# Kernel optimization log

Hardware: AMD Instinct MI355X
Metric: run time of the kernel (lower is better)

The kernel has to match this reference:

```python
import jax, jax.numpy as jnp
import numpy as np

IN_FEATURES = 8192
OUT_FEATURES = 8192
PACKED_ROWS = IN_FEATURES // 1024 * 96  # 3 uint32 words per 32 int3 values


def unpack_int3(qweight):
    """Unpack GPTQ int3 layout: each group of 3 uint32 words along the row axis
    encodes 32 int3 values for 32 consecutive in-features (per output column).
    Matches Quant3Linear.pack():
      word0: v0..v9 at bits 0,3,...,27; low 2 bits of v10 at bits 30-31
      word1: bit0 = high bit of v10; v11..v20 at bits 1,4,...,28; bit31 = low bit of v21
      word2: bits 0-1 = high 2 bits of v21; v22..v31 at bits 2,5,...,29
    Returns float32 array of shape (in_features, out_features).
    """
    out_f = qweight.shape[-1]
    q = qweight.astype(jnp.uint32).reshape(-1, 3, out_f)  # (groups, 3, out)
    w0, w1, w2 = q[:, 0], q[:, 1], q[:, 2]
    seven = jnp.uint32(7)
    vals = []
    for j in range(10):
        vals.append((w0 >> (3 * j)) & seven)
    vals.append(((w0 >> 30) & jnp.uint32(3)) | ((w1 & jnp.uint32(1)) << 2))  # v10
    for j in range(10):
        vals.append((w1 >> (3 * j + 1)) & seven)
    vals.append(((w1 >> 31) & jnp.uint32(1)) | ((w2 & jnp.uint32(3)) << 1))  # v21
    for j in range(10):
        vals.append((w2 >> (3 * j + 2)) & seven)
    w = jnp.stack(vals, axis=1)  # (groups, 32, out)
    return w.reshape(-1, out_f).astype(jnp.float32)  # (in, out)


def setup_inputs() -> dict:
    key = jax.random.key(0)
    k_x, k_q, k_s, k_z, k_b = jax.random.split(key, 5)
    x = jax.random.normal(k_x, (1, IN_FEATURES), dtype=jnp.float32)
    # random packed bits (full 32-bit entropy), stored as int32 like the torch buffer
    qweight = jax.random.bits(k_q, (PACKED_ROWS, OUT_FEATURES), dtype=jnp.uint32).astype(jnp.int32)
    scales = jax.random.uniform(k_s, (OUT_FEATURES, 1), dtype=jnp.float32, minval=0.01, maxval=0.05)
    # buffer stores zeros*scales (already pre-multiplied in pack())
    zeros = jax.random.uniform(k_z, (OUT_FEATURES, 1), dtype=jnp.float32, minval=0.0, maxval=0.2)
    bias = jax.random.normal(k_b, (OUT_FEATURES,), dtype=jnp.float32)
    return {"x": x, "qweight": qweight, "scales": scales, "zeros": zeros, "bias": bias}


def reference(x, qweight, scales, zeros, bias):
    # y[o] = bias[o] + sum_i x[i] * (scales[o] * q[i,o] - zeros[o])
    dtype = x.dtype
    q = unpack_int3(qweight)                      # (in, out) float32
    W = q * scales.T - zeros.T                    # dequantized weight (in, out)
    y = x.astype(jnp.float32) @ W + bias          # (1, out)
    return y.astype(dtype)
```

## Files before the change

### kernel.cpp

```cpp
#include <hip/hip_runtime.h>
#include <cstdint>

#define IN_F 8192
#define OUT_F 8192
#define KCHUNKS 32
#define ROWS_PER_CHUNK 24
#define KB_PER_CHUNK 8
#define COLS_PER_BLOCK 256

__global__ __launch_bounds__(256) void q3gemv(
    const float* __restrict__ x, const uint32_t* __restrict__ qw,
    const float* __restrict__ scales, const float* __restrict__ zeros,
    const float* __restrict__ bias, float* __restrict__ out)
{
    __shared__ float red[4];

    const int tid = threadIdx.x;
    const int col = blockIdx.x * COLS_PER_BLOCK + tid;
    const int kc  = blockIdx.y;

    float xv = x[kc * 256 + tid];
    float s = xv;
    #pragma unroll
    for (int off = 32; off > 0; off >>= 1)
        s += __shfl_down(s, off, 64);
    const int wid  = tid >> 6;
    const int lane = tid & 63;
    if (lane == 0) red[wid] = s;
    __syncthreads();
    const float sx_slice = red[0] + red[1] + red[2] + red[3];

    const uint32_t* qp = qw + (size_t)(kc * ROWS_PER_CHUNK) * OUT_F + col;
    const float* xb = x + kc * 256;
    float a0 = 0.f, a1 = 0.f, a2 = 0.f, a3 = 0.f;

    #pragma unroll
    for (int kb = 0; kb < KB_PER_CHUNK; ++kb) {
        const uint32_t w0 = qp[0];
        const uint32_t w1 = qp[OUT_F];
        const uint32_t w2 = qp[2 * OUT_F];
        qp += 3 * OUT_F;
        const float* xs = xb + kb * 32;

        a0 += xs[0]  * (float)( w0         & 7u);
        a1 += xs[1]  * (float)((w0 >> 3)   & 7u);
        a2 += xs[2]  * (float)((w0 >> 6)   & 7u);
        a3 += xs[3]  * (float)((w0 >> 9)   & 7u);
        a0 += xs[4]  * (float)((w0 >> 12)  & 7u);
        a1 += xs[5]  * (float)((w0 >> 15)  & 7u);
        a2 += xs[6]  * (float)((w0 >> 18)  & 7u);
        a3 += xs[7]  * (float)((w0 >> 21)  & 7u);
        a0 += xs[8]  * (float)((w0 >> 24)  & 7u);
        a1 += xs[9]  * (float)((w0 >> 27)  & 7u);
        a2 += xs[10] * (float)(((w0 >> 30) & 3u) | ((w1 & 1u) << 2));
        a3 += xs[11] * (float)((w1 >> 1)   & 7u);
        a0 += xs[12] * (float)((w1 >> 4)   & 7u);
        a1 += xs[13] * (float)((w1 >> 7)   & 7u);
        a2 += xs[14] * (float)((w1 >> 10)  & 7u);
        a3 += xs[15] * (float)((w1 >> 13)  & 7u);
        a0 += xs[16] * (float)((w1 >> 16)  & 7u);
        a1 += xs[17] * (float)((w1 >> 19)  & 7u);
        a2 += xs[18] * (float)((w1 >> 22)  & 7u);
        a3 += xs[19] * (float)((w1 >> 25)  & 7u);
        a0 += xs[20] * (float)((w1 >> 28)  & 7u);
        a1 += xs[21] * (float)(((w1 >> 31) & 1u) | ((w2 & 3u) << 1));
        a2 += xs[22] * (float)((w2 >> 2)   & 7u);
        a3 += xs[23] * (float)((w2 >> 5)   & 7u);
        a0 += xs[24] * (float)((w2 >> 8)   & 7u);
        a1 += xs[25] * (float)((w2 >> 11)  & 7u);
        a2 += xs[26] * (float)((w2 >> 14)  & 7u);
        a3 += xs[27] * (float)((w2 >> 17)  & 7u);
        a0 += xs[28] * (float)((w2 >> 20)  & 7u);
        a1 += xs[29] * (float)((w2 >> 23)  & 7u);
        a2 += xs[30] * (float)((w2 >> 26)  & 7u);
        a3 += xs[31] * (float)((w2 >> 29)  & 7u);
    }

    const float dot = (a0 + a1) + (a2 + a3);
    float v = scales[col] * dot - zeros[col] * sx_slice;
    if (kc == 0) v += bias[col];
    atomicAdd(&out[col], v);
}

extern "C" void kernel_launch(void* const* d_in, const int* in_sizes, int n_in,
                              void* d_out, int out_size, void* d_ws, size_t ws_size,
                              hipStream_t stream) {
    const float*    x      = (const float*)d_in[0];
    const uint32_t* qw     = (const uint32_t*)d_in[1];
    const float*    scales = (const float*)d_in[2];
    const float*    zeros  = (const float*)d_in[3];
    const float*    bias   = (const float*)d_in[4];
    float* out = (float*)d_out;

    hipMemsetAsync(out, 0, OUT_F * sizeof(float), stream);

    dim3 grid(OUT_F / COLS_PER_BLOCK, KCHUNKS);
    q3gemv<<<grid, 256, 0, stream>>>(x, qw, scales, zeros, bias, out);
}
```

Measured before the change: 79.69 us.

## Vectorize weight loads to four columns per thread and split K into more chunks

Each thread now handles four adjacent output columns and loads packed weights as uint4 (128-bit) loads. The K dimension is split into 64 chunks of 128 inputs instead of 32 chunks of 256, which keeps the block count the same. The per-chunk sum of x is computed with a single-wavefront xor shuffle, with no shared memory or barrier. The aim is wider memory transactions and more x reuse per thread. The costs are a single accumulator chain per column, twice as many atomics per output, and more registers per thread.

```diff
diff --git a/kernel.cpp b/kernel.cpp
--- a/kernel.cpp
+++ b/kernel.cpp
@@ -3,83 +3,97 @@
 
 #define IN_F 8192
 #define OUT_F 8192
-#define KCHUNKS 32
-#define ROWS_PER_CHUNK 24
-#define KB_PER_CHUNK 8
-#define COLS_PER_BLOCK 256
+#define KCHUNKS 64
+#define ROWS_PER_CHUNK 12
+#define KB_PER_CHUNK 4
+#define THREADS 256
+#define COLS_PER_THREAD 4
+#define COLS_PER_BLOCK (THREADS * COLS_PER_THREAD)
 
-__global__ __launch_bounds__(256) void q3gemv(
+__device__ __forceinline__ void unpack_fma(uint32_t w0, uint32_t w1, uint32_t w2,
+                                           const float* __restrict__ xs, float& a)
+{
+    a += xs[0]  * (float)( w0         & 7u);
+    a += xs[1]  * (float)((w0 >> 3)   & 7u);
+    a += xs[2]  * (float)((w0 >> 6)   & 7u);
+    a += xs[3]  * (float)((w0 >> 9)   & 7u);
+    a += xs[4]  * (float)((w0 >> 12)  & 7u);
+    a += xs[5]  * (float)((w0 >> 15)  & 7u);
+    a += xs[6]  * (float)((w0 >> 18)  & 7u);
+    a += xs[7]  * (float)((w0 >> 21)  & 7u);
+    a += xs[8]  * (float)((w0 >> 24)  & 7u);
+    a += xs[9]  * (float)((w0 >> 27)  & 7u);
+    a += xs[10] * (float)(((w0 >> 30) & 3u) | ((w1 & 1u) << 2));
+    a += xs[11] * (float)((w1 >> 1)   & 7u);
+    a += xs[12] * (float)((w1 >> 4)   & 7u);
+    a += xs[13] * (float)((w1 >> 7)   & 7u);
+    a += xs[14] * (float)((w1 >> 10)  & 7u);
+    a += xs[15] * (float)((w1 >> 13)  & 7u);
+    a += xs[16] * (float)((w1 >> 16)  & 7u);
+    a += xs[17] * (float)((w1 >> 19)  & 7u);
+    a += xs[18] * (float)((w1 >> 22)  & 7u);
+    a += xs[19] * (float)((w1 >> 25)  & 7u);
+    a += xs[20] * (float)((w1 >> 28)  & 7u);
+    a += xs[21] * (float)(((w1 >> 31) & 1u) | ((w2 & 3u) << 1));
+    a += xs[22] * (float)((w2 >> 2)   & 7u);
+    a += xs[23] * (float)((w2 >> 5)   & 7u);
+    a += xs[24] * (float)((w2 >> 8)   & 7u);
+    a += xs[25] * (float)((w2 >> 11)  & 7u);
+    a += xs[26] * (float)((w2 >> 14)  & 7u);
+    a += xs[27] * (float)((w2 >> 17)  & 7u);
+    a += xs[28] * (float)((w2 >> 20)  & 7u);
+    a += xs[29] * (float)((w2 >> 23)  & 7u);
+    a += xs[30] * (float)((w2 >> 26)  & 7u);
+    a += xs[31] * (float)((w2 >> 29)  & 7u);
+}
+
+__global__ __launch_bounds__(THREADS) void q3gemv(
     const float* __restrict__ x, const uint32_t* __restrict__ qw,
     const float* __restrict__ scales, const float* __restrict__ zeros,
     const float* __restrict__ bias, float* __restrict__ out)
 {
-    __shared__ float red[4];
+    const int tid  = threadIdx.x;
+    const int lane = tid & 63;
+    const int c0   = blockIdx.x * COLS_PER_BLOCK + tid * COLS_PER_THREAD;
+    const int kc   = blockIdx.y;
 
-    const int tid = threadIdx.x;
-    const int col = blockIdx.x * COLS_PER_BLOCK + tid;
-    const int kc  = blockIdx.y;
-
-    float xv = x[kc * 256 + tid];
-    float s = xv;
+    const float* xb = x + kc * 128;
+    float sx = xb[lane] + xb[64 + lane];
     #pragma unroll
     for (int off = 32; off > 0; off >>= 1)
-        s += __shfl_down(s, off, 64);
-    const int wid  = tid >> 6;
-    const int lane = tid & 63;
-    if (lane == 0) red[wid] = s;
-    __syncthreads();
-    const float sx_slice = red[0] + red[1] + red[2] + red[3];
+        sx += __shfl_xor(sx, off, 64);
 
-    const uint32_t* qp = qw + (size_t)(kc * ROWS_PER_CHUNK) * OUT_F + col;
-    const float* xb = x + kc * 256;
-    float a0 = 0.f, a1 = 0.f, a2 = 0.f, a3 = 0.f;
+    const uint32_t* qp = qw + (size_t)(kc * ROWS_PER_CHUNK) * OUT_F + c0;
+    float acc0 = 0.f, acc1 = 0.f, acc2 = 0.f, acc3 = 0.f;
 
     #pragma unroll
     for (int kb = 0; kb < KB_PER_CHUNK; ++kb) {
-        const uint32_t w0 = qp[0];
-        const uint32_t w1 = qp[OUT_F];
-        const uint32_t w2 = qp[2 * OUT_F];
+        const uint4 q0 = *(const uint4*)(qp);
+        const uint4 q1 = *(const uint4*)(qp + OUT_F);
+        const uint4 q2 = *(const uint4*)(qp + 2 * OUT_F);
         qp += 3 * OUT_F;
         const float* xs = xb + kb * 32;
 
-        a0 += xs[0]  * (float)( w0         & 7u);
-        a1 += xs[1]  * (float)((w0 >> 3)   & 7u);
-        a2 += xs[2]  * (float)((w0 >> 6)   & 7u);
-        a3 += xs[3]  * (float)((w0 >> 9)   & 7u);
-        a0 += xs[4]  * (float)((w0 >> 12)  & 7u);
-        a1 += xs[5]  * (float)((w0 >> 15)  & 7u);
-        a2 += xs[6]  * (float)((w0 >> 18)  & 7u);
-        a3 += xs[7]  * (float)((w0 >> 21)  & 7u);
-        a0 += xs[8]  * (float)((w0 >> 24)  & 7u);
-        a1 += xs[9]  * (float)((w0 >> 27)  & 7u);
-        a2 += xs[10] * (float)(((w0 >> 30) & 3u) | ((w1 & 1u) << 2));
-        a3 += xs[11] * (float)((w1 >> 1)   & 7u);
-        a0 += xs[12] * (float)((w1 >> 4)   & 7u);
-        a1 += xs[13] * (float)((w1 >> 7)   & 7u);
-        a2 += xs[14] * (float)((w1 >> 10)  & 7u);
-        a3 += xs[15] * (float)((w1 >> 13)  & 7u);
-        a0 += xs[16] * (float)((w1 >> 16)  & 7u);
-        a1 += xs[17] * (float)((w1 >> 19)  & 7u);
-        a2 += xs[18] * (float)((w1 >> 22)  & 7u);
-        a3 += xs[19] * (float)((w1 >> 25)  & 7u);
-        a0 += xs[20] * (float)((w1 >> 28)  & 7u);
-        a1 += xs[21] * (float)(((w1 >> 31) & 1u) | ((w2 & 3u) << 1));
-        a2 += xs[22] * (float)((w2 >> 2)   & 7u);
-        a3 += xs[23] * (float)((w2 >> 5)   & 7u);
-        a0 += xs[24] * (float)((w2 >> 8)   & 7u);
-        a1 += xs[25] * (float)((w2 >> 11)  & 7u);
-        a2 += xs[26] * (float)((w2 >> 14)  & 7u);
-        a3 += xs[27] * (float)((w2 >> 17)  & 7u);
-        a0 += xs[28] * (float)((w2 >> 20)  & 7u);
-        a1 += xs[29] * (float)((w2 >> 23)  & 7u);
-        a2 += xs[30] * (float)((w2 >> 26)  & 7u);
-        a3 += xs[31] * (float)((w2 >> 29)  & 7u);
+        unpack_fma(q0.x, q1.x, q2.x, xs, acc0);
+        unpack_fma(q0.y, q1.y, q2.y, xs, acc1);
+        unpack_fma(q0.z, q1.z, q2.z, xs, acc2);
+        unpack_fma(q0.w, q1.w, q2.w, xs, acc3);
     }
 
-    const float dot = (a0 + a1) + (a2 + a3);
-    float v = scales[col] * dot - zeros[col] * sx_slice;
-    if (kc == 0) v += bias[col];
-    atomicAdd(&out[col], v);
+    const float4 sc = *(const float4*)(scales + c0);
+    const float4 zr = *(const float4*)(zeros + c0);
+    float v0 = sc.x * acc0 - zr.x * sx;
+    float v1 = sc.y * acc1 - zr.y * sx;
+    float v2 = sc.z * acc2 - zr.z * sx;
+    float v3 = sc.w * acc3 - zr.w * sx;
+    if (kc == 0) {
+        const float4 bi = *(const float4*)(bias + c0);
+        v0 += bi.x; v1 += bi.y; v2 += bi.z; v3 += bi.w;
+    }
+    atomicAdd(&out[c0 + 0], v0);
+    atomicAdd(&out[c0 + 1], v1);
+    atomicAdd(&out[c0 + 2], v2);
+    atomicAdd(&out[c0 + 3], v3);
 }
 
 extern "C" void kernel_launch(void* const* d_in, const int* in_sizes, int n_in,
@@ -95,5 +109,5 @@
     hipMemsetAsync(out, 0, OUT_F * sizeof(float), stream);
 
     dim3 grid(OUT_F / COLS_PER_BLOCK, KCHUNKS);
-    q3gemv<<<grid, 256, 0, stream>>>(x, qw, scales, zeros, bias, out);
+    q3gemv<<<grid, THREADS, 0, stream>>>(x, qw, scales, zeros, bias, out);
 }
```

Result: slower. 88.58 us (+11.2%).

## Halve K-chunk size, front-load all packed-weight loads, drop shared-memory reduction

Applied to the files above, without the earlier changes.

Splits the reduction dimension into 64 chunks of 128 inputs instead of 32 chunks of 256, doubling the grid so more blocks are in flight. Each thread now issues all 12 of its packed-word loads up front into registers so they can all be outstanding at once. The x-sum is computed per wavefront with xor shuffles, removing the shared-memory reduction and the barrier. The cost is twice as many atomic adds to the output and a higher occupancy hint in the launch bounds.

```diff
diff --git a/kernel.cpp b/kernel.cpp
--- a/kernel.cpp
+++ b/kernel.cpp
@@ -3,44 +3,37 @@
 
 #define IN_F 8192
 #define OUT_F 8192
-#define KCHUNKS 32
-#define ROWS_PER_CHUNK 24
-#define KB_PER_CHUNK 8
-#define COLS_PER_BLOCK 256
+#define KCHUNKS 64
+#define ROWS_PER_CHUNK 12
+#define THREADS 256
 
-__global__ __launch_bounds__(256) void q3gemv(
+__global__ __launch_bounds__(THREADS, 8) void q3gemv(
     const float* __restrict__ x, const uint32_t* __restrict__ qw,
     const float* __restrict__ scales, const float* __restrict__ zeros,
     const float* __restrict__ bias, float* __restrict__ out)
 {
-    __shared__ float red[4];
+    const int tid  = threadIdx.x;
+    const int lane = tid & 63;
+    const int col  = blockIdx.x * THREADS + tid;
+    const int kc   = blockIdx.y;
 
-    const int tid = threadIdx.x;
-    const int col = blockIdx.x * COLS_PER_BLOCK + tid;
-    const int kc  = blockIdx.y;
+    const uint32_t* qp = qw + (size_t)(kc * ROWS_PER_CHUNK) * OUT_F + col;
+    uint32_t w[12];
+    #pragma unroll
+    for (int r = 0; r < 12; ++r) w[r] = qp[(size_t)r * OUT_F];
 
-    float xv = x[kc * 256 + tid];
-    float s = xv;
+    const float* xb = x + kc * 128;
+    float sx = xb[lane] + xb[64 + lane];
     #pragma unroll
     for (int off = 32; off > 0; off >>= 1)
-        s += __shfl_down(s, off, 64);
-    const int wid  = tid >> 6;
-    const int lane = tid & 63;
-    if (lane == 0) red[wid] = s;
-    __syncthreads();
-    const float sx_slice = red[0] + red[1] + red[2] + red[3];
+        sx += __shfl_xor(sx, off, 64);
 
-    const uint32_t* qp = qw + (size_t)(kc * ROWS_PER_CHUNK) * OUT_F + col;
-    const float* xb = x + kc * 256;
     float a0 = 0.f, a1 = 0.f, a2 = 0.f, a3 = 0.f;
 
     #pragma unroll
-    for (int kb = 0; kb < KB_PER_CHUNK; ++kb) {
-        const uint32_t w0 = qp[0];
-        const uint32_t w1 = qp[OUT_F];
-        const uint32_t w2 = qp[2 * OUT_F];
-        qp += 3 * OUT_F;
-        const float* xs = xb + kb * 32;
+    for (int t = 0; t < 4; ++t) {
+        const uint32_t w0 = w[3 * t], w1 = w[3 * t + 1], w2 = w[3 * t + 2];
+        const float* xs = xb + t * 32;
 
         a0 += xs[0]  * (float)( w0         & 7u);
         a1 += xs[1]  * (float)((w0 >> 3)   & 7u);
@@ -77,7 +70,7 @@
     }
 
     const float dot = (a0 + a1) + (a2 + a3);
-    float v = scales[col] * dot - zeros[col] * sx_slice;
+    float v = scales[col] * dot - zeros[col] * sx;
     if (kc == 0) v += bias[col];
     atomicAdd(&out[col], v);
 }
@@ -94,6 +87,6 @@
 
     hipMemsetAsync(out, 0, OUT_F * sizeof(float), stream);
 
-    dim3 grid(OUT_F / COLS_PER_BLOCK, KCHUNKS);
-    q3gemv<<<grid, 256, 0, stream>>>(x, qw, scales, zeros, bias, out);
+    dim3 grid(OUT_F / THREADS, KCHUNKS);
+    q3gemv<<<grid, THREADS, 0, stream>>>(x, qw, scales, zeros, bias, out);
 }
```

Result: slower. 83.88 us (+5.3%).
